# Kernel optimization log

Hardware: AMD Instinct MI355X
Metric: run time of the kernel (lower is better)

The kernel has to match this reference:

```python
import jax, jax.numpy as jnp
import numpy as np

B, C, Dz, Hh, Ww = 1, 128, 24, 24, 24
L = Dz * Hh * Ww
D_STATE = 16
D_CONV = 4
EXPAND = 2
D_INNER = EXPAND * C
DT_RANK = (C + 15) // 16  # ceil(d_model/16) = 8


def setup_inputs() -> dict:
    key = jax.random.key(0)
    ks = jax.random.split(key, 10)
    s = 0.02
    return {
        "x": jax.random.normal(ks[0], (B, C, Dz, Hh, Ww), dtype=jnp.float32),
        "ln_w": jnp.ones((C,), jnp.float32),
        "ln_b": jnp.zeros((C,), jnp.float32),
        "in_proj_w": s * jax.random.normal(ks[1], (2 * D_INNER, C), jnp.float32),
        "conv_w": s * jax.random.normal(ks[2], (D_INNER, D_CONV), jnp.float32),
        "conv_b": jnp.zeros((D_INNER,), jnp.float32),
        "x_proj_w": s * jax.random.normal(ks[3], (DT_RANK + 2 * D_STATE, D_INNER), jnp.float32),
        "dt_proj_w": s * jax.random.normal(ks[4], (D_INNER, DT_RANK), jnp.float32),
        "dt_proj_b": jax.random.uniform(ks[5], (D_INNER,), jnp.float32, -4.0, -2.0),
        "A_log": jnp.log(jnp.broadcast_to(jnp.arange(1, D_STATE + 1, dtype=jnp.float32), (D_INNER, D_STATE))),
        "D_param": jnp.ones((D_INNER,), jnp.float32),
        "out_proj_w": s * jax.random.normal(ks[6], (C, D_INNER), jnp.float32),
    }


def _mamba_forward(x, ln_w, ln_b, in_proj_w, conv_w, conv_b, x_proj_w,
                   dt_proj_w, dt_proj_b, A_log, D_param, out_proj_w):
    b, c, d, h, w = x.shape
    l = d * h * w
    tokens = x.reshape(b, c, l).transpose(0, 2, 1)  # (B,L,C)

    # LayerNorm over channel dim
    mu = jnp.mean(tokens, axis=-1, keepdims=True)
    var = jnp.var(tokens, axis=-1, keepdims=True)
    tn = (tokens - mu) * jax.lax.rsqrt(var + 1e-5) * ln_w + ln_b

    # in_proj -> x, z
    xz = jnp.einsum('blc,ec->ble', tn, in_proj_w)  # (B,L,2*d_inner)
    xs, z = jnp.split(xz, 2, axis=-1)

    # causal depthwise conv1d over L (kernel size D_CONV)
    xpad = jnp.pad(xs, ((0, 0), (D_CONV - 1, 0), (0, 0)))
    xc = conv_b
    xc = sum(xpad[:, k:k + l, :] * conv_w[:, k] for k in range(D_CONV)) + conv_b
    xa = jax.nn.silu(xc)  # (B,L,d_inner)

    # x_proj -> dt, B, C
    x_dbl = jnp.einsum('bld,ed->ble', xa, x_proj_w)
    dt_in = x_dbl[..., :DT_RANK]
    Bm = x_dbl[..., DT_RANK:DT_RANK + D_STATE]          # (B,L,d_state)
    Cm = x_dbl[..., DT_RANK + D_STATE:]                 # (B,L,d_state)
    dt = jax.nn.softplus(jnp.einsum('blr,dr->bld', dt_in, dt_proj_w) + dt_proj_b)

    A = -jnp.exp(A_log)  # (d_inner, d_state)

    def step(hst, inp):
        dt_t, B_t, C_t, x_t = inp  # (B,d_inner),(B,d_state),(B,d_state),(B,d_inner)
        dA = jnp.exp(dt_t[..., None] * A)                       # (B,d_inner,d_state)
        hst = dA * hst + (dt_t * x_t)[..., None] * B_t[:, None, :]
        y_t = jnp.einsum('bds,bs->bd', hst, C_t)
        return hst, y_t

    h0 = jnp.zeros((b, D_INNER, D_STATE), xa.dtype)
    xs_t = (dt.transpose(1, 0, 2), Bm.transpose(1, 0, 2), Cm.transpose(1, 0, 2), xa.transpose(1, 0, 2))
    _, ys = jax.lax.scan(step, h0, xs_t)
    y = ys.transpose(1, 0, 2) + xa * D_param  # (B,L,d_inner)

    y = y * jax.nn.silu(z)
    out = jnp.einsum('bld,cd->blc', y, out_proj_w)

    tokens = tokens + out
    return tokens.transpose(0, 2, 1).reshape(b, c, d, h, w)


def reference(x, ln_w, ln_b, in_proj_w, conv_w, conv_b, x_proj_w,
              dt_proj_w, dt_proj_b, A_log, D_param, out_proj_w):
    return _mamba_forward(x, ln_w, ln_b, in_proj_w, conv_w, conv_b, x_proj_w,
                          dt_proj_w, dt_proj_b, A_log, D_param, out_proj_w)
```

## Files before the change

### kernel.cpp

```cpp
#include <hip/hip_runtime.h>
#include <hip/hip_bf16.h>
#include <math.h>


constexpr int LQ = 13824;
constexpr int NC = 216;
constexpr int CH = 64;
constexpr int NB = 108;
constexpr int DI = 256;
constexpr int DS = 16;

typedef __attribute__((ext_vector_type(8))) short short8v;
typedef __attribute__((ext_vector_type(4))) float float4v;

__device__ __forceinline__ ushort f2bf(float f) {
  uint u = __float_as_uint(f);
  u += 0x7FFFu + ((u >> 16) & 1u);
  return (ushort)(u >> 16);
}
__device__ __forceinline__ float bf2f(ushort u) {
  return __uint_as_float(((uint)u) << 16);
}
__device__ __forceinline__ void gl_lds16(const ushort* g, ushort* l) {
  __builtin_amdgcn_global_load_lds(
      (const __attribute__((address_space(1))) void*)g,
      (__attribute__((address_space(3))) void*)l, 16, 0, 0);
}

template<int CTRL>
__device__ __forceinline__ float dpp_add(float x) {
  int y = __builtin_amdgcn_update_dpp(0, __float_as_int(x), CTRL, 0xF, 0xF, true);
  return x + __int_as_float(y);
}
__device__ __forceinline__ float quad_reduce(float t) {
  t = dpp_add<0xB1>(t);
  t = dpp_add<0x4E>(t);
  return t;
}
__device__ __forceinline__ float softplus_f(float x) {
  return (x > 20.f) ? x : log1pf(__expf(x));
}

__global__ __launch_bounds__(256) void prep_ln(const float* __restrict__ w_in,
    const float* __restrict__ w_xp, const float* __restrict__ w_dt,
    const float* __restrict__ w_out,
    const float* __restrict__ x, const float* __restrict__ lnw,
    const float* __restrict__ lnb,
    ushort* __restrict__ b_in, ushort* __restrict__ b_xp2, ushort* __restrict__ b_out,
    ushort* __restrict__ tn) {
  if (blockIdx.x < 704) {
    int idx = blockIdx.x * 256 + threadIdx.x;
    if (idx < 65536) {
      b_in[idx] = f2bf(w_in[idx]);
    } else if (idx < 65536 + 8192) {
      int j = idx - 65536; int r = j >> 8, k = j & 255;
      b_xp2[j] = f2bf(w_xp[(8 + r) * 256 + k]);
    } else if (idx < 65536 + 8192 + 65536) {
      int j = idx - (65536 + 8192); int d = j >> 8, k = j & 255;
      float acc = 0.f;
      #pragma unroll
      for (int r = 0; r < 8; ++r) acc += w_dt[d * 8 + r] * w_xp[r * 256 + k];
      b_xp2[8192 + j] = f2bf(acc);
    } else if (idx < 65536 + 8192 + 65536 + 8192) {
      b_xp2[73728 + (idx - 139264)] = 0;
    } else if (idx < 180224) {
      int j = idx - 147456;
      b_out[j] = f2bf(w_out[j]);
    }
  } else {
    __shared__ float red[64][8];
    __shared__ float stat[64][2];
    __shared__ ushort T[64][136];
    const int t = threadIdx.x;
    const int l = t & 63, q = t >> 6;
    const int l0 = (blockIdx.x - 704) * 64;
    float vals[32];
    float sum = 0.f, sq = 0.f;
    #pragma unroll 8
    for (int cc = 0; cc < 32; ++cc) {
      float v = x[(size_t)(q * 32 + cc) * LQ + l0 + l];
      vals[cc] = v;
      sum += v; sq += v * v;
    }
    red[l][q] = sum; red[l][4 + q] = sq;
    __syncthreads();
    if (t < 64) {
      float s  = red[t][0] + red[t][1] + red[t][2] + red[t][3];
      float s2 = red[t][4] + red[t][5] + red[t][6] + red[t][7];
      float mu = s * (1.f / 128.f);
      float var = s2 * (1.f / 128.f) - mu * mu;
      stat[t][0] = mu; stat[t][1] = rsqrtf(var + 1e-5f);
    }
    __syncthreads();
    float mu = stat[l][0], rs = stat[l][1];
    #pragma unroll 8
    for (int cc = 0; cc < 32; ++cc) {
      int c = q * 32 + cc;
      T[l][c] = f2bf((vals[cc] - mu) * rs * lnw[c] + lnb[c]);
    }
    __syncthreads();
    int row = t >> 2, seg = t & 3;
    #pragma unroll
    for (int j = 0; j < 4; ++j) {
      short8v v = *(const short8v*)&T[row][seg * 32 + j * 8];
      *(short8v*)&tn[(size_t)(l0 + row) * 128 + seg * 32 + j * 8] = v;
    }
  }
}

__global__ __launch_bounds__(256) void gemm_in_conv(
    const ushort* __restrict__ Wb,
    const ushort* __restrict__ Act,
    const float* __restrict__ cw, const float* __restrict__ cb,
    ushort* __restrict__ xa, ushort* __restrict__ zt) {
  constexpr int K = 128, KO = 16;
  __shared__ ushort As[64 * K];
  __shared__ ushort Bs[2][128 * 64];
  __shared__ __align__(16) ushort bnd[3 * 64];
  const int tid = threadIdx.x;
  const int l0 = blockIdx.x * 128;
  const int my = blockIdx.y;
  const int m0 = my * 64;
  const bool isconv = (my < 4);
  #pragma unroll
  for (int i = 0; i < 4; ++i) {
    int cid = i * 256 + tid;
    int m = cid / KO, oct = cid % KO;
    short8v v = *(const short8v*)&Wb[(size_t)(m0 + m) * K + oct * 8];
    *(short8v*)&As[m * K + ((oct ^ (m & 7)) * 8)] = v;
  }
  #pragma unroll
  for (int i = 0; i < 4; ++i) {
    int cid = i * 256 + tid;
    int l = cid >> 3, oct = (cid & 7) ^ (l & 7);
    gl_lds16(&Act[(size_t)(l0 + l) * 128 + oct * 8], &Bs[0][cid * 8]);
  }
  if (isconv && tid < 192) {
    int r = tid >> 6, m = tid & 63;
    int lg = l0 - 3 + r;
    float acc = 0.f;
    if (lg >= 0) {
      const ushort* wr = &Wb[(size_t)(m0 + m) * K];
      const ushort* tr = &Act[(size_t)lg * 128];
      for (int k = 0; k < 128; k += 8) {
        short8v wv = *(const short8v*)&wr[k];
        short8v tv = *(const short8v*)&tr[k];
        #pragma unroll
        for (int j = 0; j < 8; ++j)
          acc = fmaf(bf2f((ushort)wv[j]), bf2f((ushort)tv[j]), acc);
      }
    }
    bnd[r * 64 + m] = f2bf(acc);
  }
  float4v acc[4][2];
  #pragma unroll
  for (int a = 0; a < 4; ++a)
    #pragma unroll
    for (int b = 0; b < 2; ++b) acc[a][b] = (float4v)0.f;
  const int w = tid >> 6, lane = tid & 63;
  const int r = lane & 15, g = lane >> 4;
  int buf = 0;
  __syncthreads();
  for (int k0 = 0; k0 < K; k0 += 64) {
    if (k0 + 64 < K) {
      #pragma unroll
      for (int i = 0; i < 4; ++i) {
        int cid = i * 256 + tid;
        int l = cid >> 3, oct = (cid & 7) ^ (l & 7);
        gl_lds16(&Act[(size_t)(l0 + l) * 128 + (k0 + 64) + oct * 8],
                 &Bs[buf ^ 1][cid * 8]);
      }
    }
    const ushort* bp = Bs[buf];
    #pragma unroll
    for (int kk = 0; kk < 2; ++kk) {
      short8v af[4], bfv[2];
      int ko = (k0 >> 3) + kk * 4 + g;
      #pragma unroll
      for (int mf = 0; mf < 4; ++mf) {
        int row = mf * 16 + r;
        af[mf] = *(const short8v*)&As[row * K + ((ko ^ (row & 7)) * 8)];
      }
      int kob = kk * 4 + g;
      #pragma unroll
      for (int nf = 0; nf < 2; ++nf) {
        int row = w * 32 + nf * 16 + r;
        bfv[nf] = *(const short8v*)&bp[row * 64 + ((kob ^ (row & 7)) * 8)];
      }
      #pragma unroll
      for (int mf = 0; mf < 4; ++mf)
        #pragma unroll
        for (int nf = 0; nf < 2; ++nf)
          acc[mf][nf] = __builtin_amdgcn_mfma_f32_16x16x32_bf16(af[mf], bfv[nf], acc[mf][nf], 0, 0, 0);
    }
    __syncthreads();
    buf ^= 1;
  }
  #pragma unroll
  for (int mf = 0; mf < 4; ++mf) {
    #pragma unroll
    for (int nf = 0; nf < 2; ++nf) {
      int l = w * 32 + nf * 16 + r;
      int m = mf * 16 + g * 4;
      ushort u0 = f2bf(acc[mf][nf][0]), u1 = f2bf(acc[mf][nf][1]);
      ushort u2 = f2bf(acc[mf][nf][2]), u3 = f2bf(acc[mf][nf][3]);
      uint2 pk = make_uint2((uint)u0 | ((uint)u1 << 16), (uint)u2 | ((uint)u3 << 16));
      int oct = (m >> 3) ^ (l & 7);
      *(uint2*)&Bs[0][l * 64 + oct * 8 + (g & 1) * 4] = pk;
    }
  }
  __syncthreads();
  if (isconv) {
    const int oct_ = tid & 7;
    const int dbase = m0 + oct_ * 8;
    float w0[8], w1[8], w2[8], w3[8], bb8[8];
    #pragma unroll
    for (int j = 0; j < 8; ++j) {
      float4 wv = *(const float4*)&cw[(dbase + j) * 4];
      w0[j] = wv.x; w1[j] = wv.y; w2[j] = wv.z; w3[j] = wv.w;
      bb8[j] = cb[dbase + j];
    }
    #pragma unroll
    for (int i = 0; i < 4; ++i) {
      int cid = i * 256 + tid;
      int row = cid >> 3, oct = cid & 7;
      short8v s[4];
      #pragma unroll
      for (int t = 0; t < 4; ++t) {
        int rr = row - 3 + t;
        if (rr >= 0)
          s[t] = *(const short8v*)&Bs[0][rr * 64 + ((oct ^ (rr & 7)) * 8)];
        else
          s[t] = *(const short8v*)&bnd[(rr + 3) * 64 + oct * 8];
      }
      short8v ov;
      #pragma unroll
      for (int j = 0; j < 8; ++j) {
        float a = bb8[j] + w0[j] * bf2f((ushort)s[0][j]) + w1[j] * bf2f((ushort)s[1][j])
                         + w2[j] * bf2f((ushort)s[2][j]) + w3[j] * bf2f((ushort)s[3][j]);
        ov[j] = (short)f2bf(a / (1.f + __expf(-a)));
      }
      *(short8v*)&xa[(size_t)(l0 + row) * 256 + m0 + oct * 8] = ov;
    }
  } else {
    #pragma unroll
    for (int i = 0; i < 4; ++i) {
      int cid = i * 256 + tid;
      int row = cid >> 3, oct = cid & 7;
      short8v v = *(const short8v*)&Bs[0][row * 64 + ((oct ^ (row & 7)) * 8)];
      *(short8v*)&zt[(size_t)(l0 + row) * 256 + (m0 - 256) + oct * 8] = v;
    }
  }
}

template<int K, int MV, int BSTR, int CSTR>
__global__ __launch_bounds__(256) void gemm_tok(
    const ushort* __restrict__ Wb,
    const ushort* __restrict__ Act,
    ushort* __restrict__ Out) {
  constexpr int KO = K / 8;
  __shared__ ushort As[64 * K];
  __shared__ ushort Bs[2][128 * 64];
  const int tid = threadIdx.x;
  const int l0 = blockIdx.x * 128;
  const int m0 = blockIdx.y * 64;
  #pragma unroll
  for (int i = 0; i < (64 * KO) / 256; ++i) {
    int cid = i * 256 + tid;
    int m = cid / KO, oct = cid % KO;
    short8v v = *(const short8v*)&Wb[(size_t)(m0 + m) * K + oct * 8];
    *(short8v*)&As[m * K + ((oct ^ (m & 7)) * 8)] = v;
  }
  #pragma unroll
  for (int i = 0; i < 4; ++i) {
    int cid = i * 256 + tid;
    int l = cid >> 3, oct = (cid & 7) ^ (l & 7);
    gl_lds16(&Act[(size_t)(l0 + l) * BSTR + oct * 8], &Bs[0][cid * 8]);
  }
  float4v acc[4][2];
  #pragma unroll
  for (int a = 0; a < 4; ++a)
    #pragma unroll
    for (int b = 0; b < 2; ++b) acc[a][b] = (float4v)0.f;
  const int w = tid >> 6, lane = tid & 63;
  const int r = lane & 15, g = lane >> 4;
  int buf = 0;
  __syncthreads();
  for (int k0 = 0; k0 < K; k0 += 64) {
    if (k0 + 64 < K) {
      #pragma unroll
      for (int i = 0; i < 4; ++i) {
        int cid = i * 256 + tid;
        int l = cid >> 3, oct = (cid & 7) ^ (l & 7);
        gl_lds16(&Act[(size_t)(l0 + l) * BSTR + (k0 + 64) + oct * 8],
                 &Bs[buf ^ 1][cid * 8]);
      }
    }
    const ushort* bp = Bs[buf];
    #pragma unroll
    for (int kk = 0; kk < 2; ++kk) {
      short8v af[4], bfv[2];
      int ko = (k0 >> 3) + kk * 4 + g;
      #pragma unroll
      for (int mf = 0; mf < 4; ++mf) {
        int row = mf * 16 + r;
        af[mf] = *(const short8v*)&As[row * K + ((ko ^ (row & 7)) * 8)];
      }
      int kob = kk * 4 + g;
      #pragma unroll
      for (int nf = 0; nf < 2; ++nf) {
        int row = w * 32 + nf * 16 + r;
        bfv[nf] = *(const short8v*)&bp[row * 64 + ((kob ^ (row & 7)) * 8)];
      }
      #pragma unroll
      for (int mf = 0; mf < 4; ++mf)
        #pragma unroll
        for (int nf = 0; nf < 2; ++nf)
          acc[mf][nf] = __builtin_amdgcn_mfma_f32_16x16x32_bf16(af[mf], bfv[nf], acc[mf][nf], 0, 0, 0);
    }
    __syncthreads();
    buf ^= 1;
  }
  #pragma unroll
  for (int mf = 0; mf < 4; ++mf) {
    #pragma unroll
    for (int nf = 0; nf < 2; ++nf) {
      int l = w * 32 + nf * 16 + r;
      int m = mf * 16 + g * 4;
      ushort u0 = f2bf(acc[mf][nf][0]), u1 = f2bf(acc[mf][nf][1]);
      ushort u2 = f2bf(acc[mf][nf][2]), u3 = f2bf(acc[mf][nf][3]);
      uint2 pk = make_uint2((uint)u0 | ((uint)u1 << 16), (uint)u2 | ((uint)u3 << 16));
      int oct = (m >> 3) ^ (l & 7);
      *(uint2*)&Bs[0][l * 64 + oct * 8 + (g & 1) * 4] = pk;
    }
  }
  __syncthreads();
  #pragma unroll
  for (int i = 0; i < 4; ++i) {
    int cid = i * 256 + tid;
    int row = cid >> 3, oct = cid & 7;
    if (oct * 8 < MV) {
      short8v v = *(const short8v*)&Bs[0][row * 64 + ((oct ^ (row & 7)) * 8)];
      *(short8v*)&Out[(size_t)(l0 + row) * CSTR + m0 + oct * 8] = v;
    }
  }
}

__global__ __launch_bounds__(256) void gemm_out_k(
    const ushort* __restrict__ Wb,
    const ushort* __restrict__ Yg,
    const float* __restrict__ X,
    float* __restrict__ Out) {
  __shared__ ushort Ay[2][128 * 64];
  __shared__ ushort Bw[64 * 256];
  const int tid = threadIdx.x;
  const int l0 = blockIdx.x * 128;
  const int c0 = blockIdx.y * 64;
  const int w = tid >> 6, lane = tid & 63;
  const int r = lane & 15, g = lane >> 4;
  #pragma unroll
  for (int i = 0; i < 8; ++i) {
    int cid = i * 256 + tid;
    int row = cid >> 5, oct = cid & 31;
    short8v vb = *(const short8v*)&Wb[(size_t)(c0 + row) * 256 + oct * 8];
    *(short8v*)&Bw[row * 256 + ((oct ^ (row & 7)) * 8)] = vb;
  }
  #pragma unroll
  for (int i = 0; i < 4; ++i) {
    int cid = i * 256 + tid;
    int row = cid >> 3, oct = (cid & 7) ^ (row & 7);
    gl_lds16(&Yg[((size_t)(oct >> 1) * LQ + l0 + row) * 16 + (oct & 1) * 8],
             &Ay[0][cid * 8]);
  }
  float4v acc[2][4];
  #pragma unroll
  for (int a = 0; a < 2; ++a)
    #pragma unroll
    for (int b = 0; b < 4; ++b) acc[a][b] = (float4v)0.f;
  int buf = 0;
  __syncthreads();
  for (int k0 = 0; k0 < 256; k0 += 64) {
    if (k0 + 64 < 256) {
      int ks = (k0 + 64) >> 4;
      #pragma unroll
      for (int i = 0; i < 4; ++i) {
        int cid = i * 256 + tid;
        int row = cid >> 3, oct = (cid & 7) ^ (row & 7);
        gl_lds16(&Yg[((size_t)(ks + (oct >> 1)) * LQ + l0 + row) * 16 + (oct & 1) * 8],
                 &Ay[buf ^ 1][cid * 8]);
      }
    }
    const ushort* ap = Ay[buf];
    #pragma unroll
    for (int kk = 0; kk < 2; ++kk) {
      int kob = kk * 4 + g;
      int ko = (k0 >> 3) + kob;
      short8v af[2], bfv[4];
      #pragma unroll
      for (int mf = 0; mf < 2; ++mf) {
        int row = w * 32 + mf * 16 + r;
        af[mf] = *(const short8v*)&ap[row * 64 + ((kob ^ (row & 7)) * 8)];
      }
      #pragma unroll
      for (int nf = 0; nf < 4; ++nf) {
        int row = nf * 16 + r;
        bfv[nf] = *(const short8v*)&Bw[row * 256 + ((ko ^ (row & 7)) * 8)];
      }
      #pragma unroll
      for (int mf = 0; mf < 2; ++mf)
        #pragma unroll
        for (int nf = 0; nf < 4; ++nf)
          acc[mf][nf] = __builtin_amdgcn_mfma_f32_16x16x32_bf16(af[mf], bfv[nf], acc[mf][nf], 0, 0, 0);
    }
    __syncthreads();
    buf ^= 1;
  }
  #pragma unroll
  for (int mf = 0; mf < 2; ++mf) {
    #pragma unroll
    for (int nf = 0; nf < 4; ++nf) {
      int c = c0 + nf * 16 + r;
      int l = l0 + w * 32 + mf * 16 + g * 4;
      size_t off = (size_t)c * LQ + l;
      float4 rv = *(const float4*)&X[off];
      float4 o = make_float4(acc[mf][nf][0] + rv.x, acc[mf][nf][1] + rv.y,
                             acc[mf][nf][2] + rv.z, acc[mf][nf][3] + rv.w);
      *(float4*)&Out[off] = o;
    }
  }
}

__global__ __launch_bounds__(256) void scan1(const ushort* __restrict__ xdbl,
    const ushort* __restrict__ xa, const float* __restrict__ bias,
    const float* __restrict__ A_log, float* __restrict__ Stot, float* __restrict__ Hc,
    ushort* __restrict__ yloc) {
  __shared__ uint  duL[64 * 64];
  __shared__ float bcL[64 * 32];
  __shared__ ushort ylds[64 * 72];
  const int tid = threadIdx.x;
  const int c = blockIdx.x, dg = blockIdx.y;
  const int dloc = tid >> 2, sq = tid & 3;
  const int d = dg * 64 + dloc;
  const int lb = c * CH;
  float4v A, h;
  #pragma unroll
  for (int k = 0; k < 4; ++k) {
    A[k] = -__expf(A_log[d * 16 + sq * 4 + k]);
    h[k] = 0.f;
  }
  float S = 0.f;
  {
    const int doff = dg * 64 + sq * 16;
    const ushort* xr = xdbl + (size_t)(lb + dloc) * 320 + 32 + doff;
    const ushort* xar = xa + (size_t)(lb + dloc) * 256 + doff;
    short8v d0 = *(const short8v*)xr;
    short8v d1 = *(const short8v*)(xr + 8);
    short8v x0 = *(const short8v*)xar;
    short8v x1 = *(const short8v*)(xar + 8);
    uint pk[16];
    #pragma unroll
    for (int j = 0; j < 8; ++j) {
      float sp = softplus_f(bf2f((ushort)d0[j]) + bias[doff + j]);
      pk[j] = (uint)f2bf(sp) | ((uint)f2bf(sp * bf2f((ushort)x0[j])) << 16);
      float sp2 = softplus_f(bf2f((ushort)d1[j]) + bias[doff + 8 + j]);
      pk[8 + j] = (uint)f2bf(sp2) | ((uint)f2bf(sp2 * bf2f((ushort)x1[j])) << 16);
    }
    uint4* dst = (uint4*)&duL[dloc * 64 + sq * 16];
    #pragma unroll
    for (int j = 0; j < 4; ++j)
      dst[j] = make_uint4(pk[4 * j], pk[4 * j + 1], pk[4 * j + 2], pk[4 * j + 3]);
  }
  if (tid < 128) {
    int row = tid >> 1, half = tid & 1;
    const ushort* xr = xdbl + (size_t)(lb + row) * 320;
    short8v bv = *(const short8v*)(xr + half * 8);
    short8v cv = *(const short8v*)(xr + 16 + half * 8);
    float* bd = &bcL[row * 32 + half * 8];
    float* cd = &bcL[row * 32 + 16 + half * 8];
    #pragma unroll
    for (int j = 0; j < 8; ++j) {
      bd[j] = bf2f((ushort)bv[j]);
      cd[j] = bf2f((ushort)cv[j]);
    }
  }
  __syncthreads();
  #pragma unroll 4
  for (int i = 0; i < CH; ++i) {
    uint pv = duL[i * 64 + dloc];
    float dtv = __uint_as_float(pv << 16);
    float dxv = __uint_as_float(pv & 0xffff0000u);
    S += dtv;
    float4v Bv = *(const float4v*)&bcL[i * 32 + sq * 4];
    float4v Cv = *(const float4v*)&bcL[i * 32 + 16 + sq * 4];
    float t = 0.f;
    #pragma unroll
    for (int k = 0; k < 4; ++k) {
      float a = __expf(dtv * A[k]);
      h[k] = fmaf(a, h[k], dxv * Bv[k]);
      t = fmaf(h[k], Cv[k], t);
    }
    t = quad_reduce(t);
    if (sq == 0) ylds[i * 72 + dloc] = f2bf(t);
  }
  __syncthreads();
  {
    int slab = tid >> 6, row = tid & 63;
    short8v v0 = *(const short8v*)&ylds[row * 72 + slab * 16];
    short8v v1 = *(const short8v*)&ylds[row * 72 + slab * 16 + 8];
    ushort* dst = &yloc[((size_t)(dg * 4 + slab) * LQ + lb + row) * 16];
    *(short8v*)dst = v0;
    *(short8v*)(dst + 8) = v1;
  }
  *(float4*)&Hc[(size_t)(c * 256 + d) * 16 + sq * 4] = make_float4(h[0], h[1], h[2], h[3]);
  if (sq == 0) Stot[c * 256 + d] = S;
}

__global__ __launch_bounds__(256) void scan_combine(const float* __restrict__ Stot,
    const float* __restrict__ Hc, const float* __restrict__ A_log,
    float* __restrict__ Hin) {
  int t = blockIdx.x * 256 + threadIdx.x;
  int d = t >> 4;
  float A = -__expf(A_log[t]);
  float h = 0.f;
  for (int cb = 0; cb < NC; cb += 8) {
    float a[8], b[8];
    #pragma unroll
    for (int j = 0; j < 8; ++j) {
      a[j] = Stot[(cb + j) * 256 + d];
      b[j] = Hc[(size_t)(cb + j) * 4096 + t];
    }
    #pragma unroll
    for (int j = 0; j < 8; ++j) {
      Hin[(size_t)(cb + j) * 4096 + t] = h;
      h = fmaf(__expf(A * a[j]), h, b[j]);
    }
  }
}

__global__ __launch_bounds__(256) void scan2(const ushort* __restrict__ xdbl,
    const ushort* __restrict__ xa, const ushort* __restrict__ zt,
    const float* __restrict__ bias, const float* __restrict__ A_log,
    const float* __restrict__ Dp, const float* __restrict__ Hin,
    ushort* __restrict__ yg) {
  __shared__ uint  dtp[32 * 64];
  __shared__ float cL[64 * 16];
  __shared__ float corr[64 * 68];
  const int tid = threadIdx.x;
  const int c = blockIdx.x, dg = blockIdx.y;
  const int dloc = tid >> 2, sq = tid & 3;
  const int d = dg * 64 + dloc;
  const int lb = c * CH;
  float4v A, hin;
  #pragma unroll
  for (int k = 0; k < 4; ++k) A[k] = -__expf(A_log[d * 16 + sq * 4 + k]);
  {
    float4 hv = *(const float4*)&Hin[(size_t)(c * 256 + d) * 16 + sq * 4];
    hin[0] = hv.x; hin[1] = hv.y; hin[2] = hv.z; hin[3] = hv.w;
  }
  float S = 0.f;
  {
    int rp = tid >> 3, seg = tid & 7;
    const int doff = dg * 64 + seg * 8;
    const ushort* xr0 = xdbl + (size_t)(lb + 2 * rp) * 320 + 32 + doff;
    short8v e0 = *(const short8v*)xr0;
    short8v e1 = *(const short8v*)(xr0 + 320);
    uint pk[8];
    #pragma unroll
    for (int j = 0; j < 8; ++j) {
      float spe = softplus_f(bf2f((ushort)e0[j]) + bias[doff + j]);
      float spo = softplus_f(bf2f((ushort)e1[j]) + bias[doff + j]);
      pk[j] = (uint)f2bf(spe) | ((uint)f2bf(spo) << 16);
    }
    uint4* dst = (uint4*)&dtp[rp * 64 + seg * 8];
    dst[0] = make_uint4(pk[0], pk[1], pk[2], pk[3]);
    dst[1] = make_uint4(pk[4], pk[5], pk[6], pk[7]);
  }
  if (tid < 128) {
    int row = tid >> 1, half = tid & 1;
    short8v cv = *(const short8v*)(xdbl + (size_t)(lb + row) * 320 + 16 + half * 8);
    float* cd = &cL[row * 16 + half * 8];
    #pragma unroll
    for (int j = 0; j < 8; ++j) cd[j] = bf2f((ushort)cv[j]);
  }
  __syncthreads();
  #pragma unroll 2
  for (int i2 = 0; i2 < CH / 2; ++i2) {
    uint pv = dtp[i2 * 64 + dloc];
    #pragma unroll
    for (int par = 0; par < 2; ++par) {
      float dtv = (par == 0) ? __uint_as_float(pv << 16)
                             : __uint_as_float(pv & 0xffff0000u);
      S += dtv;
      int i = i2 * 2 + par;
      float4v Cv = *(const float4v*)&cL[i * 16 + sq * 4];
      float t = 0.f;
      #pragma unroll
      for (int k = 0; k < 4; ++k)
        t = fmaf(__expf(A[k] * S), hin[k] * Cv[k], t);
      t = quad_reduce(t);
      if (sq == 0) corr[i * 68 + dloc] = t;
    }
  }
  __syncthreads();
  {
    int slab = tid >> 6, row = tid & 63;
    const int doff = dg * 64 + slab * 16;
    size_t sl = ((size_t)(dg * 4 + slab) * LQ + lb + row) * 16;
    short8v y0 = *(const short8v*)&yg[sl];
    short8v y1 = *(const short8v*)&yg[sl + 8];
    const ushort* xav = xa + (size_t)(lb + row) * 256 + doff;
    short8v x0 = *(const short8v*)xav;
    short8v x1 = *(const short8v*)(xav + 8);
    const ushort* zvp = zt + (size_t)(lb + row) * 256 + doff;
    short8v z0 = *(const short8v*)zvp;
    short8v z1 = *(const short8v*)(zvp + 8);
    float4 c0 = *(const float4*)&corr[row * 68 + slab * 16];
    float4 c1 = *(const float4*)&corr[row * 68 + slab * 16 + 4];
    float4 c2 = *(const float4*)&corr[row * 68 + slab * 16 + 8];
    float4 c3 = *(const float4*)&corr[row * 68 + slab * 16 + 12];
    float cr[16] = {c0.x, c0.y, c0.z, c0.w, c1.x, c1.y, c1.z, c1.w,
                    c2.x, c2.y, c2.z, c2.w, c3.x, c3.y, c3.z, c3.w};
    short8v o0, o1;
    #pragma unroll
    for (int j = 0; j < 8; ++j) {
      float v0 = bf2f((ushort)y0[j]) + cr[j] + bf2f((ushort)x0[j]) * Dp[doff + j];
      float zf0 = bf2f((ushort)z0[j]);
      o0[j] = (short)f2bf(v0 * (zf0 / (1.f + __expf(-zf0))));
      float v1 = bf2f((ushort)y1[j]) + cr[8 + j] + bf2f((ushort)x1[j]) * Dp[doff + 8 + j];
      float zf1 = bf2f((ushort)z1[j]);
      o1[j] = (short)f2bf(v1 * (zf1 / (1.f + __expf(-zf1))));
    }
    *(short8v*)&yg[sl] = o0;
    *(short8v*)&yg[sl + 8] = o1;
  }
}

extern "C" void kernel_launch(void* const* d_in, const int* in_sizes, int n_in,
                              void* d_out, int out_size, void* d_ws, size_t ws_size,
                              hipStream_t stream) {
  const float* x         = (const float*)d_in[0];
  const float* ln_w      = (const float*)d_in[1];
  const float* ln_b      = (const float*)d_in[2];
  const float* in_proj_w = (const float*)d_in[3];
  const float* conv_w    = (const float*)d_in[4];
  const float* conv_b    = (const float*)d_in[5];
  const float* x_proj_w  = (const float*)d_in[6];
  const float* dt_proj_w = (const float*)d_in[7];
  const float* dt_proj_b = (const float*)d_in[8];
  const float* A_log     = (const float*)d_in[9];
  const float* D_param   = (const float*)d_in[10];
  const float* out_proj_w= (const float*)d_in[11];
  float* out = (float*)d_out;

  char* ws = (char*)d_ws;
  ushort* wbf_in  = (ushort*)(ws + 0);
  ushort* wbf_xp2 = (ushort*)(ws + 131072);
  ushort* wbf_out = (ushort*)(ws + 294912);
  float*  Hin     = (float*)(ws + 360448);
  float*  Hc      = (float*)(ws + 3899392);
  float*  Stot    = (float*)(ws + 7438336);
  ushort* tn_t    = (ushort*)(ws + 7659520);
  ushort* zt      = (ushort*)(ws + 11198464);
  ushort* xa_t    = (ushort*)(ws + 18276352);
  ushort* xdbl_t  = (ushort*)(ws + 25354240);
  ushort* yg_t    = (ushort*)(ws + 34201600);

  prep_ln<<<920, 256, 0, stream>>>(in_proj_w, x_proj_w, dt_proj_w, out_proj_w,
                                   x, ln_w, ln_b, wbf_in, wbf_xp2, wbf_out, tn_t);
  gemm_in_conv<<<dim3(NB, 8), 256, 0, stream>>>(wbf_in, tn_t, conv_w, conv_b, xa_t, zt);
  gemm_tok<256, 64, 256, 320><<<dim3(NB, 5), 256, 0, stream>>>(wbf_xp2, xa_t, xdbl_t);
  scan1<<<dim3(NC, 4), 256, 0, stream>>>(xdbl_t, xa_t, dt_proj_b, A_log, Stot, Hc, yg_t);
  scan_combine<<<16, 256, 0, stream>>>(Stot, Hc, A_log, Hin);
  scan2<<<dim3(NC, 4), 256, 0, stream>>>(xdbl_t, xa_t, zt, dt_proj_b, A_log,
                                         D_param, Hin, yg_t);
  gemm_out_k<<<dim3(NB, 2), 256, 0, stream>>>(wbf_out, yg_t, x, out);
}
```

Baseline: 203.0 us.

## Stream weight tiles via double-buffered async LDS loads and shrink scan2 correction buffer

The two token GEMMs used to load the whole weight panel into shared memory up front through registers. They now stream 64-wide K slices of the weights with async global-to-LDS loads, double-buffered alongside the activation tiles. This cuts LDS use, which may raise occupancy, and overlaps the weight loads with MFMA work. scan2 also stores its correction term in bf16 with a padded stride, halving that LDS buffer at some cost in precision.

```diff
diff --git a/kernel.cpp b/kernel.cpp
--- a/kernel.cpp
+++ b/kernel.cpp
@@ -258,18 +258,16 @@
     const ushort* __restrict__ Wb,
     const ushort* __restrict__ Act,
     ushort* __restrict__ Out) {
-  constexpr int KO = K / 8;
-  __shared__ ushort As[64 * K];
+  __shared__ ushort As[2][64 * 64];
   __shared__ ushort Bs[2][128 * 64];
   const int tid = threadIdx.x;
   const int l0 = blockIdx.x * 128;
   const int m0 = blockIdx.y * 64;
   #pragma unroll
-  for (int i = 0; i < (64 * KO) / 256; ++i) {
+  for (int i = 0; i < 2; ++i) {
     int cid = i * 256 + tid;
-    int m = cid / KO, oct = cid % KO;
-    short8v v = *(const short8v*)&Wb[(size_t)(m0 + m) * K + oct * 8];
-    *(short8v*)&As[m * K + ((oct ^ (m & 7)) * 8)] = v;
+    int m = cid >> 3, oct = (cid & 7) ^ (m & 7);
+    gl_lds16(&Wb[(size_t)(m0 + m) * K + oct * 8], &As[0][cid * 8]);
   }
   #pragma unroll
   for (int i = 0; i < 4; ++i) {
@@ -288,6 +286,12 @@
   __syncthreads();
   for (int k0 = 0; k0 < K; k0 += 64) {
     if (k0 + 64 < K) {
+      #pragma unroll
+      for (int i = 0; i < 2; ++i) {
+        int cid = i * 256 + tid;
+        int m = cid >> 3, oct = (cid & 7) ^ (m & 7);
+        gl_lds16(&Wb[(size_t)(m0 + m) * K + (k0 + 64) + oct * 8], &As[buf ^ 1][cid * 8]);
+      }
       #pragma unroll
       for (int i = 0; i < 4; ++i) {
         int cid = i * 256 + tid;
@@ -296,17 +300,17 @@
                  &Bs[buf ^ 1][cid * 8]);
       }
     }
+    const ushort* ap = As[buf];
     const ushort* bp = Bs[buf];
     #pragma unroll
     for (int kk = 0; kk < 2; ++kk) {
       short8v af[4], bfv[2];
-      int ko = (k0 >> 3) + kk * 4 + g;
+      int kob = kk * 4 + g;
       #pragma unroll
       for (int mf = 0; mf < 4; ++mf) {
         int row = mf * 16 + r;
-        af[mf] = *(const short8v*)&As[row * K + ((ko ^ (row & 7)) * 8)];
-      }
-      int kob = kk * 4 + g;
+        af[mf] = *(const short8v*)&ap[row * 64 + ((kob ^ (row & 7)) * 8)];
+      }
       #pragma unroll
       for (int nf = 0; nf < 2; ++nf) {
         int row = w * 32 + nf * 16 + r;
@@ -352,18 +356,17 @@
     const float* __restrict__ X,
     float* __restrict__ Out) {
   __shared__ ushort Ay[2][128 * 64];
-  __shared__ ushort Bw[64 * 256];
+  __shared__ ushort Bw[2][64 * 64];
   const int tid = threadIdx.x;
   const int l0 = blockIdx.x * 128;
   const int c0 = blockIdx.y * 64;
   const int w = tid >> 6, lane = tid & 63;
   const int r = lane & 15, g = lane >> 4;
   #pragma unroll
-  for (int i = 0; i < 8; ++i) {
+  for (int i = 0; i < 2; ++i) {
     int cid = i * 256 + tid;
-    int row = cid >> 5, oct = cid & 31;
-    short8v vb = *(const short8v*)&Wb[(size_t)(c0 + row) * 256 + oct * 8];
-    *(short8v*)&Bw[row * 256 + ((oct ^ (row & 7)) * 8)] = vb;
+    int row = cid >> 3, oct = (cid & 7) ^ (row & 7);
+    gl_lds16(&Wb[(size_t)(c0 + row) * 256 + oct * 8], &Bw[0][cid * 8]);
   }
   #pragma unroll
   for (int i = 0; i < 4; ++i) {
@@ -383,6 +386,12 @@
     if (k0 + 64 < 256) {
       int ks = (k0 + 64) >> 4;
       #pragma unroll
+      for (int i = 0; i < 2; ++i) {
+        int cid = i * 256 + tid;
+        int row = cid >> 3, oct = (cid & 7) ^ (row & 7);
+        gl_lds16(&Wb[(size_t)(c0 + row) * 256 + (k0 + 64) + oct * 8], &Bw[buf ^ 1][cid * 8]);
+      }
+      #pragma unroll
       for (int i = 0; i < 4; ++i) {
         int cid = i * 256 + tid;
         int row = cid >> 3, oct = (cid & 7) ^ (row & 7);
@@ -391,10 +400,10 @@
       }
     }
     const ushort* ap = Ay[buf];
+    const ushort* bp = Bw[buf];
     #pragma unroll
     for (int kk = 0; kk < 2; ++kk) {
       int kob = kk * 4 + g;
-      int ko = (k0 >> 3) + kob;
       short8v af[2], bfv[4];
       #pragma unroll
       for (int mf = 0; mf < 2; ++mf) {
@@ -404,7 +413,7 @@
       #pragma unroll
       for (int nf = 0; nf < 4; ++nf) {
         int row = nf * 16 + r;
-        bfv[nf] = *(const short8v*)&Bw[row * 256 + ((ko ^ (row & 7)) * 8)];
+        bfv[nf] = *(const short8v*)&bp[row * 64 + ((kob ^ (row & 7)) * 8)];
       }
       #pragma unroll
       for (int mf = 0; mf < 2; ++mf)
@@ -544,7 +553,7 @@
     ushort* __restrict__ yg) {
   __shared__ uint  dtp[32 * 64];
   __shared__ float cL[64 * 16];
-  __shared__ float corr[64 * 68];
+  __shared__ ushort corr[64 * 72];
   const int tid = threadIdx.x;
   const int c = blockIdx.x, dg = blockIdx.y;
   const int dloc = tid >> 2, sq = tid & 3;
@@ -598,7 +607,7 @@
       for (int k = 0; k < 4; ++k)
         t = fmaf(__expf(A[k] * S), hin[k] * Cv[k], t);
       t = quad_reduce(t);
-      if (sq == 0) corr[i * 68 + dloc] = t;
+      if (sq == 0) corr[i * 72 + dloc] = f2bf(t);
     }
   }
   __syncthreads();
@@ -614,19 +623,15 @@
     const ushort* zvp = zt + (size_t)(lb + row) * 256 + doff;
     short8v z0 = *(const short8v*)zvp;
     short8v z1 = *(const short8v*)(zvp + 8);
-    float4 c0 = *(const float4*)&corr[row * 68 + slab * 16];
-    float4 c1 = *(const float4*)&corr[row * 68 + slab * 16 + 4];
-    float4 c2 = *(const float4*)&corr[row * 68 + slab * 16 + 8];
-    float4 c3 = *(const float4*)&corr[row * 68 + slab * 16 + 12];
-    float cr[16] = {c0.x, c0.y, c0.z, c0.w, c1.x, c1.y, c1.z, c1.w,
-                    c2.x, c2.y, c2.z, c2.w, c3.x, c3.y, c3.z, c3.w};
+    short8v c0 = *(const short8v*)&corr[row * 72 + slab * 16];
+    short8v c1 = *(const short8v*)&corr[row * 72 + slab * 16 + 8];
     short8v o0, o1;
     #pragma unroll
     for (int j = 0; j < 8; ++j) {
-      float v0 = bf2f((ushort)y0[j]) + cr[j] + bf2f((ushort)x0[j]) * Dp[doff + j];
+      float v0 = bf2f((ushort)y0[j]) + bf2f((ushort)c0[j]) + bf2f((ushort)x0[j]) * Dp[doff + j];
       float zf0 = bf2f((ushort)z0[j]);
       o0[j] = (short)f2bf(v0 * (zf0 / (1.f + __expf(-zf0))));
-      float v1 = bf2f((ushort)y1[j]) + cr[8 + j] + bf2f((ushort)x1[j]) * Dp[doff + 8 + j];
+      float v1 = bf2f((ushort)y1[j]) + bf2f((ushort)c1[j]) + bf2f((ushort)x1[j]) * Dp[doff + 8 + j];
       float zf1 = bf2f((ushort)z1[j]);
       o1[j] = (short)f2bf(v1 * (zf1 / (1.f + __expf(-zf1))));
     }
```

After: 200.0 us. Within noise of the previous version (-1.5%).
